# Kernel tuning notes

Hardware: AMD Instinct MI355X
Metric: run time of the kernel (lower is better)

Reference implementation:

```python
import jax, jax.numpy as jnp
import numpy as np

B, T, C, H, FF = 4, 2048, 768, 12, 3072
D = C // H
EPS = 1e-5


def setup_inputs() -> dict:
    key = jax.random.key(0)
    ks = jax.random.split(key, 8)
    s = 0.02
    return {
        "x": jax.random.normal(ks[0], (B, T, C), jnp.float32),
        "ln1_w": jnp.ones((C,), jnp.float32),
        "ln1_b": jnp.zeros((C,), jnp.float32),
        "qkv_w": jax.random.normal(ks[1], (C, 3 * C), jnp.float32) * s,
        "qkv_b": jnp.zeros((3 * C,), jnp.float32),
        "out_w": jax.random.normal(ks[2], (C, C), jnp.float32) * s,
        "out_b": jnp.zeros((C,), jnp.float32),
        "ln2_w": jnp.ones((C,), jnp.float32),
        "ln2_b": jnp.zeros((C,), jnp.float32),
        "ff1_w": jax.random.normal(ks[3], (C, FF), jnp.float32) * s,
        "ff1_b": jnp.zeros((FF,), jnp.float32),
        "ff2_w": jax.random.normal(ks[4], (FF, C), jnp.float32) * s,
        "ff2_b": jnp.zeros((C,), jnp.float32),
    }


def _layernorm(x, w, b):
    m = jnp.mean(x, axis=-1, keepdims=True)
    v = jnp.mean(jnp.square(x - m), axis=-1, keepdims=True)
    return (x - m) * jax.lax.rsqrt(v + EPS) * w + b


def reference(x, ln1_w, ln1_b, qkv_w, qkv_b, out_w, out_b,
              ln2_w, ln2_b, ff1_w, ff1_b, ff2_w, ff2_b):
    # --- attention sublayer ---
    h = _layernorm(x, ln1_w, ln1_b)
    qkv = h @ qkv_w + qkv_b                      # [B,T,3C]
    q, k, v = jnp.split(qkv, 3, axis=-1)
    q = q.reshape(B, T, H, D)
    k = k.reshape(B, T, H, D)
    v = v.reshape(B, T, H, D)
    scores = jnp.einsum('bthd,bshd->bhts', q, k) / np.sqrt(D).astype(np.float32)
    causal = jnp.tril(jnp.ones((T, T), bool))    # [T,T]
    scores = jnp.where(causal[None, None], scores, -jnp.inf)
    attn = jax.nn.softmax(scores, axis=-1)       # [B,H,T,T]
    o = jnp.einsum('bhts,bshd->bthd', attn, v).reshape(B, T, C)
    x = x + o @ out_w + out_b
    # --- FFN sublayer ---
    h2 = _layernorm(x, ln2_w, ln2_b)
    x = x + jax.nn.relu(h2 @ ff1_w + ff1_b) @ ff2_w + ff2_b
    return x
```

## Files before the change

kernel.cpp:

```cpp
#include <hip/hip_runtime.h>
#include <hip/hip_bf16.h>
#include <cstdint>
#include <cstddef>

#define B_ 4
#define T_ 2048
#define C_ 768
#define H_ 12
#define D_ 64
#define FF_ 3072

typedef __attribute__((ext_vector_type(4))) float f32x4;
typedef __attribute__((ext_vector_type(8))) short s16x8;
typedef __attribute__((ext_vector_type(4))) short s16x4;

static __device__ __forceinline__ short f2bf(float f) {
  union { float fv; unsigned u; } v; v.fv = f;
  unsigned r = v.u + 0x7FFFu + ((v.u >> 16) & 1u);
  return (short)(r >> 16);
}

static __device__ __forceinline__ unsigned pkbf2(float a, float b) {
  __hip_bfloat162 h = __float22bfloat162_rn(make_float2(a, b));
  union { __hip_bfloat162 h2; unsigned u; } v; v.h2 = h;
  return v.u;
}

__global__ __launch_bounds__(256) void wconv(const float* __restrict__ in,
                                             short* __restrict__ out,
                                             int K, int N) {
  __shared__ float tile[32][33];
  int tk = blockIdx.x * 32, tn = blockIdx.y * 32;
  int lx = threadIdx.x & 31, ly = threadIdx.x >> 5;
#pragma unroll
  for (int i = 0; i < 4; ++i)
    tile[ly + i * 8][lx] = in[(size_t)(tk + ly + i * 8) * N + tn + lx];
  __syncthreads();
#pragma unroll
  for (int i = 0; i < 4; ++i)
    out[(size_t)(tn + ly + i * 8) * K + tk + lx] = f2bf(tile[lx][ly + i * 8]);
}

__global__ __launch_bounds__(256) void ln_kernel(const float* __restrict__ x,
                                                 const float* __restrict__ w,
                                                 const float* __restrict__ b,
                                                 short* __restrict__ out) {
  int row = blockIdx.x, tid = threadIdx.x;
  const float* xr = x + (size_t)row * 768;
  float v0 = xr[tid], v1 = xr[tid + 256], v2 = xr[tid + 512];
  float s = v0 + v1 + v2;
#pragma unroll
  for (int o = 32; o > 0; o >>= 1) s += __shfl_down(s, o);
  __shared__ float r1[4], r2[4];
  if ((tid & 63) == 0) r1[tid >> 6] = s;
  __syncthreads();
  float mean = (r1[0] + r1[1] + r1[2] + r1[3]) * (1.f / 768.f);
  float d0 = v0 - mean, d1 = v1 - mean, d2 = v2 - mean;
  float q = d0 * d0 + d1 * d1 + d2 * d2;
#pragma unroll
  for (int o = 32; o > 0; o >>= 1) q += __shfl_down(q, o);
  if ((tid & 63) == 0) r2[tid >> 6] = q;
  __syncthreads();
  float var = (r2[0] + r2[1] + r2[2] + r2[3]) * (1.f / 768.f);
  float rstd = rsqrtf(var + 1e-5f);
  short* orow = out + (size_t)row * 768;
  orow[tid]       = f2bf(d0 * rstd * w[tid]       + b[tid]);
  orow[tid + 256] = f2bf(d1 * rstd * w[tid + 256] + b[tid + 256]);
  orow[tid + 512] = f2bf(d2 * rstd * w[tid + 512] + b[tid + 512]);
}

template <int MODE>
__global__ __launch_bounds__(256) void gemm_bt(
    const short* __restrict__ A, const short* __restrict__ Bt,
    const float* __restrict__ bias, const float* __restrict__ res,
    void* __restrict__ out,
    short* __restrict__ dq, short* __restrict__ dk, short* __restrict__ dv,
    int M, int N, int K) {
  __shared__ short As[2][128 * 32];
  __shared__ short Bs[2][128 * 32];
  int tid = threadIdx.x;
  int lane = tid & 63;
  int wm = tid >> 7;
  int wn = (tid >> 6) & 1;
  const short* Ab = A + (size_t)blockIdx.x * 128 * K;
  const short* Bb = Bt + (size_t)blockIdx.y * 128 * K;
  f32x4 acc[4][4] = {};
  int i15 = lane & 15, g8 = (lane >> 4) << 3;
  int nk = K >> 6;
  for (int kt = 0; kt < nk; ++kt) {
    int kof = kt << 6;
#pragma unroll
    for (int i = 0; i < 4; ++i) {
      int s = tid + i * 256;
      int pan = s >> 9, sp = s & 511;
      int row = sp >> 2, kk = ((sp & 3) << 3) + (pan << 5);
      __builtin_amdgcn_global_load_lds(
          (const __attribute__((address_space(1))) unsigned*)(Ab + (size_t)row * K + kof + kk),
          (__attribute__((address_space(3))) unsigned*)(&As[pan][sp * 8]), 16, 0, 0);
      __builtin_amdgcn_global_load_lds(
          (const __attribute__((address_space(1))) unsigned*)(Bb + (size_t)row * K + kof + kk),
          (__attribute__((address_space(3))) unsigned*)(&Bs[pan][sp * 8]), 16, 0, 0);
    }
    __syncthreads();
#pragma unroll
    for (int h = 0; h < 2; ++h) {
      s16x8 af[4], bfr[4];
#pragma unroll
      for (int m = 0; m < 4; ++m)
        af[m] = *(const s16x8*)(&As[h][(wm * 64 + m * 16 + i15) * 32 + g8]);
#pragma unroll
      for (int n = 0; n < 4; ++n)
        bfr[n] = *(const s16x8*)(&Bs[h][(wn * 64 + n * 16 + i15) * 32 + g8]);
#pragma unroll
      for (int m = 0; m < 4; ++m)
#pragma unroll
        for (int n = 0; n < 4; ++n)
          acc[m][n] = __builtin_amdgcn_mfma_f32_16x16x32_bf16(af[m], bfr[n], acc[m][n], 0, 0, 0);
    }
    __syncthreads();
  }
  int row0 = blockIdx.x * 128 + wm * 64;
  int col0 = blockIdx.y * 128 + wn * 64;
  int g4 = (lane >> 4) << 2;
#pragma unroll
  for (int m = 0; m < 4; ++m) {
#pragma unroll
    for (int n = 0; n < 4; ++n) {
      int col = col0 + n * 16 + i15;
      float bv = bias[col];
      float v4[4];
#pragma unroll
      for (int r = 0; r < 4; ++r) v4[r] = acc[m][n][r] + bv;
      int rbase = row0 + m * 16 + g4;
      if constexpr (MODE == 0) {
        int sect = col / 768;
        int wi = col - sect * 768;
        int hh = wi >> 6, dd = wi & 63;
        int bb = rbase >> 11, tt = rbase & 2047;
        if (sect == 2) {
          s16x4 o4;
#pragma unroll
          for (int r = 0; r < 4; ++r) o4[r] = f2bf(v4[r]);
          *(s16x4*)(dv + ((size_t)(bb * H_ + hh) * D_ + dd) * T_ + tt) = o4;
        } else {
          short* dst = (sect == 0 ? dq : dk) + ((size_t)(bb * H_ + hh) * T_ + tt) * D_ + dd;
          float sc = sect == 0 ? 0.18033688f : 1.f;
#pragma unroll
          for (int r = 0; r < 4; ++r) dst[(size_t)r * D_] = f2bf(v4[r] * sc);
        }
      } else {
#pragma unroll
        for (int r = 0; r < 4; ++r)
          ((short*)out)[(size_t)(rbase + r) * N + col] = f2bf(v4[r] > 0.f ? v4[r] : 0.f);
      }
    }
  }
}

__global__ __launch_bounds__(128, 3) void gemm64_res(
    const short* __restrict__ A, const short* __restrict__ Bt,
    const float* __restrict__ bias, const float* __restrict__ res,
    float* __restrict__ out, int M, int N, int K) {
  __shared__ short As[2][64 * 32];
  __shared__ short Bs[2][128 * 32];
  int tid = threadIdx.x;
  int lane = tid & 63;
  int wn = tid >> 6;
  const short* Ab = A + (size_t)blockIdx.x * 64 * K;
  const short* Bb = Bt + (size_t)blockIdx.y * 128 * K;
  f32x4 acc[4][4] = {};
  int i15 = lane & 15, g8 = (lane >> 4) << 3;
  int nk = K >> 6;
  for (int kt = 0; kt < nk; ++kt) {
    int kof = kt << 6;
#pragma unroll
    for (int i = 0; i < 4; ++i) {
      int c = tid + i * 128;
      int pan = c >> 8, sp = c & 255;
      int row = sp >> 2, kk = ((sp & 3) << 3) + (pan << 5);
      __builtin_amdgcn_global_load_lds(
          (const __attribute__((address_space(1))) unsigned*)(Ab + (size_t)row * K + kof + kk),
          (__attribute__((address_space(3))) unsigned*)(&As[pan][sp * 8]), 16, 0, 0);
    }
#pragma unroll
    for (int i = 0; i < 8; ++i) {
      int c = tid + i * 128;
      int pan = c >> 9, sp = c & 511;
      int row = sp >> 2, kk = ((sp & 3) << 3) + (pan << 5);
      __builtin_amdgcn_global_load_lds(
          (const __attribute__((address_space(1))) unsigned*)(Bb + (size_t)row * K + kof + kk),
          (__attribute__((address_space(3))) unsigned*)(&Bs[pan][sp * 8]), 16, 0, 0);
    }
    __syncthreads();
#pragma unroll
    for (int h = 0; h < 2; ++h) {
      s16x8 af[4], bfr[4];
#pragma unroll
      for (int m = 0; m < 4; ++m)
        af[m] = *(const s16x8*)(&As[h][(m * 16 + i15) * 32 + g8]);
#pragma unroll
      for (int n = 0; n < 4; ++n)
        bfr[n] = *(const s16x8*)(&Bs[h][(wn * 64 + n * 16 + i15) * 32 + g8]);
#pragma unroll
      for (int m = 0; m < 4; ++m)
#pragma unroll
        for (int n = 0; n < 4; ++n)
          acc[m][n] = __builtin_amdgcn_mfma_f32_16x16x32_bf16(af[m], bfr[n], acc[m][n], 0, 0, 0);
    }
    __syncthreads();
  }
  int row0 = blockIdx.x * 64;
  int col0 = blockIdx.y * 128 + wn * 64;
  int g4 = (lane >> 4) << 2;
#pragma unroll
  for (int m = 0; m < 4; ++m) {
#pragma unroll
    for (int n = 0; n < 4; ++n) {
      int col = col0 + n * 16 + i15;
      float bv = bias[col];
      int rbase = row0 + m * 16 + g4;
#pragma unroll
      for (int r = 0; r < 4; ++r)
        out[(size_t)(rbase + r) * N + col] =
            acc[m][n][r] + bv + res[(size_t)(rbase + r) * N + col];
    }
  }
}

__global__ __launch_bounds__(128) void attn_kernel(const short* __restrict__ Qb,
                                                   const short* __restrict__ Kb,
                                                   const short* __restrict__ VTb,
                                                   short* __restrict__ Ob) {
  int i = blockIdx.x;
  int c = i & 7, j = i >> 3;
  int bx = j & 15, gy = j >> 4;
  int bh = c + (gy << 3);
  int bb = bh / H_, hh = bh - bb * H_;
  int tid = threadIdx.x, lane = tid & 63, wv = tid >> 6;
  int sq = (bx << 1) | wv;
  const short* Qp = Qb + (size_t)bh * T_ * D_;
  const short* Kp = Kb + (size_t)bh * T_ * D_;
  const short* Vp = VTb + (size_t)bh * D_ * T_;
  int i15 = lane & 15, g = lane >> 4, g8 = g << 3;
  int keyA0 = ((i15 >> 2) << 3) + (i15 & 3);
#pragma unroll 1
  for (int pass = 0; pass < 2; ++pass) {
    int ss = pass ? 63 - sq : sq;
    int wq0 = ss << 5;
    int nt = ss + 1;
    s16x8 qf[2][2];
#pragma unroll
    for (int s = 0; s < 2; ++s) {
      int qrow = wq0 + s * 16 + i15;
      qf[s][0] = *(const s16x8*)(Qp + (size_t)qrow * D_ + g8);
      qf[s][1] = *(const s16x8*)(Qp + (size_t)qrow * D_ + 32 + g8);
    }
    f32x4 oacc[2][4] = {};
    float lsum[2] = {0.f, 0.f};
    s16x8 ka0, ka1, kb0, kb1, va0, va1, va2, va3;
    {
      const short* KA = Kp + (size_t)keyA0 * D_;
      ka0 = *(const s16x8*)(KA + g8);
      ka1 = *(const s16x8*)(KA + 32 + g8);
      const short* KB = KA + 4 * D_;
      kb0 = *(const s16x8*)(KB + g8);
      kb1 = *(const s16x8*)(KB + 32 + g8);
      va0 = *(const s16x8*)(Vp + (size_t)(0 * 16 + i15) * T_ + g8);
      va1 = *(const s16x8*)(Vp + (size_t)(1 * 16 + i15) * T_ + g8);
      va2 = *(const s16x8*)(Vp + (size_t)(2 * 16 + i15) * T_ + g8);
      va3 = *(const s16x8*)(Vp + (size_t)(3 * 16 + i15) * T_ + g8);
    }
#pragma unroll 2
    for (int kt = 0; kt < nt; ++kt) {
      int k0 = kt << 5;
      bool last = (kt == nt - 1);
      int kn = last ? 0 : (k0 + 32);
      const short* KA = Kp + (size_t)(kn + keyA0) * D_;
      s16x8 nka0 = *(const s16x8*)(KA + g8);
      s16x8 nka1 = *(const s16x8*)(KA + 32 + g8);
      const short* KB = KA + 4 * D_;
      s16x8 nkb0 = *(const s16x8*)(KB + g8);
      s16x8 nkb1 = *(const s16x8*)(KB + 32 + g8);
      s16x8 nva0 = *(const s16x8*)(Vp + (size_t)(0 * 16 + i15) * T_ + kn + g8);
      s16x8 nva1 = *(const s16x8*)(Vp + (size_t)(1 * 16 + i15) * T_ + kn + g8);
      s16x8 nva2 = *(const s16x8*)(Vp + (size_t)(2 * 16 + i15) * T_ + kn + g8);
      s16x8 nva3 = *(const s16x8*)(Vp + (size_t)(3 * 16 + i15) * T_ + kn + g8);
#pragma unroll
      for (int s = 0; s < 2; ++s) {
        f32x4 sA = {}, sB = {};
        __builtin_amdgcn_s_setprio(1);
        sA = __builtin_amdgcn_mfma_f32_16x16x32_bf16(ka0, qf[s][0], sA, 0, 0, 0);
        sA = __builtin_amdgcn_mfma_f32_16x16x32_bf16(ka1, qf[s][1], sA, 0, 0, 0);
        sB = __builtin_amdgcn_mfma_f32_16x16x32_bf16(kb0, qf[s][0], sB, 0, 0, 0);
        sB = __builtin_amdgcn_mfma_f32_16x16x32_bf16(kb1, qf[s][1], sB, 0, 0, 0);
        __builtin_amdgcn_s_setprio(0);
        int qrow = wq0 + s * 16 + i15;
        int kb = k0 + g8;
        float sa[8];
        if (last) {
#pragma unroll
          for (int r = 0; r < 4; ++r) {
            sa[r]     = (kb + r     <= qrow) ? sA[r] : -1e30f;
            sa[4 + r] = (kb + 4 + r <= qrow) ? sB[r] : -1e30f;
          }
        } else {
#pragma unroll
          for (int r = 0; r < 4; ++r) { sa[r] = sA[r]; sa[4 + r] = sB[r]; }
        }
        float p[8];
        float ps = 0.f;
#pragma unroll
        for (int r = 0; r < 8; ++r) {
          p[r] = exp2f(sa[r]);
          ps += p[r];
        }
        lsum[s] += ps;
        union { unsigned u[4]; s16x8 v; } pf;
        pf.u[0] = pkbf2(p[0], p[1]);
        pf.u[1] = pkbf2(p[2], p[3]);
        pf.u[2] = pkbf2(p[4], p[5]);
        pf.u[3] = pkbf2(p[6], p[7]);
        __builtin_amdgcn_s_setprio(1);
        oacc[s][0] = __builtin_amdgcn_mfma_f32_16x16x32_bf16(va0, pf.v, oacc[s][0], 0, 0, 0);
        oacc[s][1] = __builtin_amdgcn_mfma_f32_16x16x32_bf16(va1, pf.v, oacc[s][1], 0, 0, 0);
        oacc[s][2] = __builtin_amdgcn_mfma_f32_16x16x32_bf16(va2, pf.v, oacc[s][2], 0, 0, 0);
        oacc[s][3] = __builtin_amdgcn_mfma_f32_16x16x32_bf16(va3, pf.v, oacc[s][3], 0, 0, 0);
        __builtin_amdgcn_s_setprio(0);
      }
      ka0 = nka0; ka1 = nka1; kb0 = nkb0; kb1 = nkb1;
      va0 = nva0; va1 = nva1; va2 = nva2; va3 = nva3;
    }
#pragma unroll
    for (int s = 0; s < 2; ++s) {
      float l = lsum[s];
      l += __shfl_xor(l, 16);
      l += __shfl_xor(l, 32);
      float inv = 1.f / l;
      int qrow = wq0 + s * 16 + i15;
      short* op = Ob + ((size_t)(bb * T_ + qrow)) * C_ + hh * D_ + (g << 2);
#pragma unroll
      for (int mt = 0; mt < 4; ++mt) {
        s16x4 o4;
#pragma unroll
        for (int r = 0; r < 4; ++r) o4[r] = f2bf(oacc[s][mt][r] * inv);
        *(s16x4*)(op + mt * 16) = o4;
      }
    }
  }
}

extern "C" void kernel_launch(void* const* d_in, const int* in_sizes, int n_in,
                              void* d_out, int out_size, void* d_ws, size_t ws_size,
                              hipStream_t stream) {
  const float* x     = (const float*)d_in[0];
  const float* ln1_w = (const float*)d_in[1];
  const float* ln1_b = (const float*)d_in[2];
  const float* qkv_w = (const float*)d_in[3];
  const float* qkv_b = (const float*)d_in[4];
  const float* out_w = (const float*)d_in[5];
  const float* out_b = (const float*)d_in[6];
  const float* ln2_w = (const float*)d_in[7];
  const float* ln2_b = (const float*)d_in[8];
  const float* ff1_w = (const float*)d_in[9];
  const float* ff1_b = (const float*)d_in[10];
  const float* ff2_w = (const float*)d_in[11];
  const float* ff2_b = (const float*)d_in[12];

  char* ws = (char*)d_ws;
  short* Wqkv = (short*)(ws + 0);
  short* Wout = (short*)(ws + 3538944);
  short* Wff1 = (short*)(ws + 4718592);
  short* Wff2 = (short*)(ws + 9437184);
  short* Hbuf = (short*)(ws + 14155776);
  short* Qb   = (short*)(ws + 26738688);
  short* Kb   = Qb + 6291456;
  short* VT   = Kb + 6291456;
  short* Ob   = VT + 6291456;
  short* FFH  = Qb;
  float* xout = (float*)d_out;

  wconv<<<dim3(24, 72), 256, 0, stream>>>(qkv_w, Wqkv, 768, 2304);
  wconv<<<dim3(24, 24), 256, 0, stream>>>(out_w, Wout, 768, 768);
  wconv<<<dim3(24, 96), 256, 0, stream>>>(ff1_w, Wff1, 768, 3072);
  wconv<<<dim3(96, 24), 256, 0, stream>>>(ff2_w, Wff2, 3072, 768);

  ln_kernel<<<8192, 256, 0, stream>>>(x, ln1_w, ln1_b, Hbuf);
  gemm_bt<0><<<dim3(64, 18), 256, 0, stream>>>(Hbuf, Wqkv, qkv_b, nullptr, nullptr,
                                               Qb, Kb, VT, 8192, 2304, 768);
  attn_kernel<<<768, 128, 0, stream>>>(Qb, Kb, VT, Ob);
  gemm64_res<<<dim3(128, 6), 128, 0, stream>>>(Ob, Wout, out_b, x, xout, 8192, 768, 768);
  ln_kernel<<<8192, 256, 0, stream>>>(xout, ln2_w, ln2_b, Hbuf);
  gemm_bt<2><<<dim3(64, 24), 256, 0, stream>>>(Hbuf, Wff1, ff1_b, nullptr, FFH,
                                               nullptr, nullptr, nullptr, 8192, 3072, 768);
  gemm64_res<<<dim3(128, 6), 128, 0, stream>>>(FFH, Wff2, ff2_b, xout, xout, 8192, 768, 3072);
}
```

Baseline: 308.1 us.

## Share K/V tiles across four waves via double-buffered LDS in attention

The attention kernel moves from per-wave register streaming of K/V out of global memory to a 256-thread block with 64 query rows. K and V tiles of 64 keys are staged into swizzled, double-buffered LDS with global_load_lds and shared by all four waves. The old two-pass causal balancing is replaced by a reversed block order that schedules the heaviest query blocks first. This cuts redundant global/L2 traffic for K/V, at the cost of a block barrier on every tile and load imbalance between blocks.

```diff
diff --git a/kernel.cpp b/kernel.cpp
--- a/kernel.cpp
+++ b/kernel.cpp
@@ -227,77 +227,87 @@
   }
 }
 
-__global__ __launch_bounds__(128) void attn_kernel(const short* __restrict__ Qb,
+__global__ __launch_bounds__(256) void attn_kernel(const short* __restrict__ Qb,
                                                    const short* __restrict__ Kb,
                                                    const short* __restrict__ VTb,
                                                    short* __restrict__ Ob) {
+  __shared__ short Ks[2][4096];
+  __shared__ short Vs[2][4096];
   int i = blockIdx.x;
   int c = i & 7, j = i >> 3;
-  int bx = j & 15, gy = j >> 4;
+  int qb = 31 - (j & 31);
+  int gy = j >> 5;
   int bh = c + (gy << 3);
   int bb = bh / H_, hh = bh - bb * H_;
   int tid = threadIdx.x, lane = tid & 63, wv = tid >> 6;
-  int sq = (bx << 1) | wv;
+  int q0 = qb << 6;
+  int nt = qb + 1;
   const short* Qp = Qb + (size_t)bh * T_ * D_;
   const short* Kp = Kb + (size_t)bh * T_ * D_;
   const short* Vp = VTb + (size_t)bh * D_ * T_;
   int i15 = lane & 15, g = lane >> 4, g8 = g << 3;
   int keyA0 = ((i15 >> 2) << 3) + (i15 & 3);
+  int keyB0 = keyA0 + 4;
+  int fA = (keyA0 & 7) ^ ((keyA0 & 8) >> 1);
+  int fB = (keyB0 & 7) ^ ((keyB0 & 8) >> 1);
+  int fV = (i15 & 7) ^ ((i15 & 8) >> 1);
+  int oA[2], oB[2], oV[2];
+#pragma unroll
+  for (int h = 0; h < 2; ++h) {
+    oA[h] = keyA0 * 64 + (((h * 4 + g) ^ fA) << 3);
+    oB[h] = keyB0 * 64 + (((h * 4 + g) ^ fB) << 3);
+    oV[h] = i15 * 64 + (((h * 4 + g) ^ fV) << 3);
+  }
+  int qrow = q0 + wv * 16 + i15;
+  s16x8 qf0 = *(const s16x8*)(Qp + (size_t)qrow * D_ + g8);
+  s16x8 qf1 = *(const s16x8*)(Qp + (size_t)qrow * D_ + 32 + g8);
+  f32x4 oacc[4] = {};
+  float lsum = 0.f;
+
+  auto stage = [&](int buf, int t) {
+    int k0 = t << 6;
+#pragma unroll
+    for (int qq = 0; qq < 2; ++qq) {
+      int m = tid + qq * 256;
+      int r = m >> 3, cd = m & 7;
+      int cs = cd ^ ((r & 7) ^ ((r & 8) >> 1));
+      __builtin_amdgcn_global_load_lds(
+          (const __attribute__((address_space(1))) unsigned*)(Kp + (size_t)(k0 + r) * D_ + (cs << 3)),
+          (__attribute__((address_space(3))) unsigned*)(&Ks[buf][m * 8]), 16, 0, 0);
+      __builtin_amdgcn_global_load_lds(
+          (const __attribute__((address_space(1))) unsigned*)(Vp + (size_t)r * T_ + k0 + (cs << 3)),
+          (__attribute__((address_space(3))) unsigned*)(&Vs[buf][m * 8]), 16, 0, 0);
+    }
+  };
+
+  stage(0, 0);
+  __syncthreads();
+  int cur = 0;
 #pragma unroll 1
-  for (int pass = 0; pass < 2; ++pass) {
-    int ss = pass ? 63 - sq : sq;
-    int wq0 = ss << 5;
-    int nt = ss + 1;
-    s16x8 qf[2][2];
-#pragma unroll
-    for (int s = 0; s < 2; ++s) {
-      int qrow = wq0 + s * 16 + i15;
-      qf[s][0] = *(const s16x8*)(Qp + (size_t)qrow * D_ + g8);
-      qf[s][1] = *(const s16x8*)(Qp + (size_t)qrow * D_ + 32 + g8);
-    }
-    f32x4 oacc[2][4] = {};
-    float lsum[2] = {0.f, 0.f};
-    s16x8 ka0, ka1, kb0, kb1, va0, va1, va2, va3;
-    {
-      const short* KA = Kp + (size_t)keyA0 * D_;
-      ka0 = *(const s16x8*)(KA + g8);
-      ka1 = *(const s16x8*)(KA + 32 + g8);
-      const short* KB = KA + 4 * D_;
-      kb0 = *(const s16x8*)(KB + g8);
-      kb1 = *(const s16x8*)(KB + 32 + g8);
-      va0 = *(const s16x8*)(Vp + (size_t)(0 * 16 + i15) * T_ + g8);
-      va1 = *(const s16x8*)(Vp + (size_t)(1 * 16 + i15) * T_ + g8);
-      va2 = *(const s16x8*)(Vp + (size_t)(2 * 16 + i15) * T_ + g8);
-      va3 = *(const s16x8*)(Vp + (size_t)(3 * 16 + i15) * T_ + g8);
-    }
-#pragma unroll 2
-    for (int kt = 0; kt < nt; ++kt) {
-      int k0 = kt << 5;
-      bool last = (kt == nt - 1);
-      int kn = last ? 0 : (k0 + 32);
-      const short* KA = Kp + (size_t)(kn + keyA0) * D_;
-      s16x8 nka0 = *(const s16x8*)(KA + g8);
-      s16x8 nka1 = *(const s16x8*)(KA + 32 + g8);
-      const short* KB = KA + 4 * D_;
-      s16x8 nkb0 = *(const s16x8*)(KB + g8);
-      s16x8 nkb1 = *(const s16x8*)(KB + 32 + g8);
-      s16x8 nva0 = *(const s16x8*)(Vp + (size_t)(0 * 16 + i15) * T_ + kn + g8);
-      s16x8 nva1 = *(const s16x8*)(Vp + (size_t)(1 * 16 + i15) * T_ + kn + g8);
-      s16x8 nva2 = *(const s16x8*)(Vp + (size_t)(2 * 16 + i15) * T_ + kn + g8);
-      s16x8 nva3 = *(const s16x8*)(Vp + (size_t)(3 * 16 + i15) * T_ + kn + g8);
-#pragma unroll
-      for (int s = 0; s < 2; ++s) {
+  for (int t = 0; t < nt; ++t) {
+    if (t + 1 < nt) stage(cur ^ 1, t + 1);
+    const short* KB = &Ks[cur][0];
+    const short* VB = &Vs[cur][0];
+    bool diag = (t == nt - 1);
+    int k0 = t << 6;
+#pragma unroll
+    for (int ks = 0; ks < 2; ++ks) {
+      if (!(ks == 1 && diag && wv < 2)) {
+        s16x8 ka0 = *(const s16x8*)(KB + (ks << 11) + oA[0]);
+        s16x8 ka1 = *(const s16x8*)(KB + (ks << 11) + oA[1]);
+        s16x8 kb0 = *(const s16x8*)(KB + (ks << 11) + oB[0]);
+        s16x8 kb1 = *(const s16x8*)(KB + (ks << 11) + oB[1]);
         f32x4 sA = {}, sB = {};
         __builtin_amdgcn_s_setprio(1);
-        sA = __builtin_amdgcn_mfma_f32_16x16x32_bf16(ka0, qf[s][0], sA, 0, 0, 0);
-        sA = __builtin_amdgcn_mfma_f32_16x16x32_bf16(ka1, qf[s][1], sA, 0, 0, 0);
-        sB = __builtin_amdgcn_mfma_f32_16x16x32_bf16(kb0, qf[s][0], sB, 0, 0, 0);
-        sB = __builtin_amdgcn_mfma_f32_16x16x32_bf16(kb1, qf[s][1], sB, 0, 0, 0);
+        sA = __builtin_amdgcn_mfma_f32_16x16x32_bf16(ka0, qf0, sA, 0, 0, 0);
+        sA = __builtin_amdgcn_mfma_f32_16x16x32_bf16(ka1, qf1, sA, 0, 0, 0);
+        sB = __builtin_amdgcn_mfma_f32_16x16x32_bf16(kb0, qf0, sB, 0, 0, 0);
+        sB = __builtin_amdgcn_mfma_f32_16x16x32_bf16(kb1, qf1, sB, 0, 0, 0);
         __builtin_amdgcn_s_setprio(0);
-        int qrow = wq0 + s * 16 + i15;
-        int kb = k0 + g8;
+        int kb = k0 + (ks << 5) + g8;
         float sa[8];
-        if (last) {
+        bool needmask = diag && ((wv < 2) == (ks == 0));
+        if (needmask) {
 #pragma unroll
           for (int r = 0; r < 4; ++r) {
             sa[r]     = (kb + r     <= qrow) ? sA[r] : -1e30f;
@@ -314,38 +324,38 @@
           p[r] = exp2f(sa[r]);
           ps += p[r];
         }
-        lsum[s] += ps;
+        lsum += ps;
         union { unsigned u[4]; s16x8 v; } pf;
         pf.u[0] = pkbf2(p[0], p[1]);
         pf.u[1] = pkbf2(p[2], p[3]);
         pf.u[2] = pkbf2(p[4], p[5]);
         pf.u[3] = pkbf2(p[6], p[7]);
+        s16x8 vf0 = *(const s16x8*)(VB + 0    + oV[ks]);
+        s16x8 vf1 = *(const s16x8*)(VB + 1024 + oV[ks]);
+        s16x8 vf2 = *(const s16x8*)(VB + 2048 + oV[ks]);
+        s16x8 vf3 = *(const s16x8*)(VB + 3072 + oV[ks]);
         __builtin_amdgcn_s_setprio(1);
-        oacc[s][0] = __builtin_amdgcn_mfma_f32_16x16x32_bf16(va0, pf.v, oacc[s][0], 0, 0, 0);
-        oacc[s][1] = __builtin_amdgcn_mfma_f32_16x16x32_bf16(va1, pf.v, oacc[s][1], 0, 0, 0);
-        oacc[s][2] = __builtin_amdgcn_mfma_f32_16x16x32_bf16(va2, pf.v, oacc[s][2], 0, 0, 0);
-        oacc[s][3] = __builtin_amdgcn_mfma_f32_16x16x32_bf16(va3, pf.v, oacc[s][3], 0, 0, 0);
+        oacc[0] = __builtin_amdgcn_mfma_f32_16x16x32_bf16(vf0, pf.v, oacc[0], 0, 0, 0);
+        oacc[1] = __builtin_amdgcn_mfma_f32_16x16x32_bf16(vf1, pf.v, oacc[1], 0, 0, 0);
+        oacc[2] = __builtin_amdgcn_mfma_f32_16x16x32_bf16(vf2, pf.v, oacc[2], 0, 0, 0);
+        oacc[3] = __builtin_amdgcn_mfma_f32_16x16x32_bf16(vf3, pf.v, oacc[3], 0, 0, 0);
         __builtin_amdgcn_s_setprio(0);
       }
-      ka0 = nka0; ka1 = nka1; kb0 = nkb0; kb1 = nkb1;
-      va0 = nva0; va1 = nva1; va2 = nva2; va3 = nva3;
-    }
-#pragma unroll
-    for (int s = 0; s < 2; ++s) {
-      float l = lsum[s];
-      l += __shfl_xor(l, 16);
-      l += __shfl_xor(l, 32);
-      float inv = 1.f / l;
-      int qrow = wq0 + s * 16 + i15;
-      short* op = Ob + ((size_t)(bb * T_ + qrow)) * C_ + hh * D_ + (g << 2);
-#pragma unroll
-      for (int mt = 0; mt < 4; ++mt) {
-        s16x4 o4;
-#pragma unroll
-        for (int r = 0; r < 4; ++r) o4[r] = f2bf(oacc[s][mt][r] * inv);
-        *(s16x4*)(op + mt * 16) = o4;
-      }
-    }
+    }
+    __syncthreads();
+    cur ^= 1;
+  }
+  float l = lsum;
+  l += __shfl_xor(l, 16);
+  l += __shfl_xor(l, 32);
+  float inv = 1.f / l;
+  short* op = Ob + ((size_t)(bb * T_ + qrow)) * C_ + hh * D_ + (g << 2);
+#pragma unroll
+  for (int mt = 0; mt < 4; ++mt) {
+    s16x4 o4;
+#pragma unroll
+    for (int r = 0; r < 4; ++r) o4[r] = f2bf(oacc[mt][r] * inv);
+    *(s16x4*)(op + mt * 16) = o4;
   }
 }
 
@@ -387,7 +397,7 @@
   ln_kernel<<<8192, 256, 0, stream>>>(x, ln1_w, ln1_b, Hbuf);
   gemm_bt<0><<<dim3(64, 18), 256, 0, stream>>>(Hbuf, Wqkv, qkv_b, nullptr, nullptr,
                                                Qb, Kb, VT, 8192, 2304, 768);
-  attn_kernel<<<768, 128, 0, stream>>>(Qb, Kb, VT, Ob);
+  attn_kernel<<<1536, 256, 0, stream>>>(Qb, Kb, VT, Ob);
   gemm64_res<<<dim3(128, 6), 128, 0, stream>>>(Ob, Wout, out_b, x, xout, 8192, 768, 768);
   ln_kernel<<<8192, 256, 0, stream>>>(xout, ln2_w, ln2_b, Hbuf);
   gemm_bt<2><<<dim3(64, 24), 256, 0, stream>>>(Hbuf, Wff1, ff1_b, nullptr, FFH,
```

Result: faster. 288.4 us (-6.4%).
